# Optimization experiments

Measured on AMD Instinct MI355X. Metric: run time of the kernel, lower is better.

Reference implementation:

```python
import jax, jax.numpy as jnp
import numpy as np

B, S, D = 2, 2048, 1024
H = 16
HD = D // H  # 64, per-head size
EPS = 1e-5


def _ln(x, g, b):
    mu = jnp.mean(x, axis=-1, keepdims=True)
    var = jnp.var(x, axis=-1, keepdims=True)
    return (x - mu) * jax.lax.rsqrt(var + EPS) * g + b


def setup_inputs() -> dict:
    key = jax.random.key(0)
    ks = jax.random.split(key, 8)
    sd = 1.0 / np.sqrt(D)
    return {
        "x": jax.random.normal(ks[0], (B, S, D), jnp.float32),
        "w_qkv": jax.random.normal(ks[1], (3 * D, D), jnp.float32) * sd,
        "w_proj": jax.random.normal(ks[2], (D, D), jnp.float32) * sd,
        "b_proj": jnp.zeros((D,), jnp.float32),
        "w1": jax.random.normal(ks[3], (4 * D, D), jnp.float32) * sd,
        "b1": jnp.zeros((4 * D,), jnp.float32),
        "w2": jax.random.normal(ks[4], (D, 4 * D), jnp.float32) * (1.0 / np.sqrt(4 * D)),
        "b2": jnp.zeros((D,), jnp.float32),
        "ln1_g": jnp.ones((D,), jnp.float32),
        "ln1_b": jnp.zeros((D,), jnp.float32),
        "ln2_g": jnp.ones((D,), jnp.float32),
        "ln2_b": jnp.zeros((D,), jnp.float32),
    }


def reference(x, w_qkv, w_proj, b_proj, w1, b1, w2, b2, ln1_g, ln1_b, ln2_g, ln2_b):
    # --- pre-LN self-attention ---
    h = _ln(x, ln1_g, ln1_b)
    qkv = jnp.einsum("bsd,ed->bse", h, w_qkv)  # [B,S,3D]
    q, k, v = jnp.split(qkv, 3, axis=-1)
    # [B,H,S,HD]
    q = q.reshape(B, S, H, HD).transpose(0, 2, 1, 3)
    k = k.reshape(B, S, H, HD).transpose(0, 2, 1, 3)
    v = v.reshape(B, S, H, HD).transpose(0, 2, 1, 3)
    logits = jnp.einsum("bhqd,bhkd->bhqk", q, k) / np.sqrt(HD)
    probs = jax.nn.softmax(logits, axis=-1)  # no causal mask in non-flash path
    out = jnp.einsum("bhqk,bhkd->bhqd", probs, v)
    out = out.transpose(0, 2, 1, 3).reshape(B, S, D)
    out = jnp.einsum("bsd,ed->bse", out, w_proj) + b_proj
    x = x + out
    # --- pre-LN MLP ---
    h2 = _ln(x, ln2_g, ln2_b)
    h2 = jax.nn.relu(jnp.einsum("bsd,fd->bsf", h2, w1) + b1)
    h2 = jnp.einsum("bsf,df->bsd", h2, w2) + b2
    return x + h2
```

## Files before the change

kernel.cpp:

```cpp
#include <hip/hip_runtime.h>
#include <stdint.h>

typedef unsigned short ushort_t;
typedef __attribute__((ext_vector_type(8))) short s16x8;
typedef __attribute__((ext_vector_type(4))) float f32x4;

static __device__ __forceinline__ float bf2f(ushort_t u) {
  union { unsigned int i; float f; } x; x.i = ((unsigned int)u) << 16; return x.f;
}
static __device__ __forceinline__ ushort_t f2bf(float f) {
  union { float f; unsigned int i; } x; x.f = f;
  unsigned int r = (x.i + 0x7FFFu + ((x.i >> 16) & 1u)) >> 16;
  return (ushort_t)r;
}
static __device__ __forceinline__ unsigned f2bf_pos_u(float f) {
  return (__float_as_uint(f) + 0x8000u) >> 16;
}
static __device__ __forceinline__ bool nonfin(float f) {
  return (__float_as_uint(f) & 0x7F800000u) == 0x7F800000u;
}

static __device__ __forceinline__ float dpp_add16(float x) {
  float y;
  y = __int_as_float(__builtin_amdgcn_update_dpp(0, __float_as_int(x), 0xB1, 0xF, 0xF, true)); x += y;
  y = __int_as_float(__builtin_amdgcn_update_dpp(0, __float_as_int(x), 0x4E, 0xF, 0xF, true)); x += y;
  y = __int_as_float(__builtin_amdgcn_update_dpp(0, __float_as_int(x), 0x141, 0xF, 0xF, true)); x += y;
  y = __int_as_float(__builtin_amdgcn_update_dpp(0, __float_as_int(x), 0x140, 0xF, 0xF, true)); x += y;
  return x;
}

#define GLL16(gp, lp) __builtin_amdgcn_global_load_lds( \
    (const __attribute__((address_space(1))) void*)(gp), \
    (__attribute__((address_space(3))) void*)(lp), 16, 0, 0)

__global__ void zero_flags(int* flags) { if (threadIdx.x < 16) flags[threadIdx.x] = 0; }

__global__ void apply_flags(const int* __restrict__ flags, float* __restrict__ out) {
  int i = threadIdx.x;
  if (i < 7 && flags[i]) out[i] = 1.0e5f * (i + 1);
}

__global__ __launch_bounds__(256) void cvt2(
    const float* __restrict__ a, ushort_t* __restrict__ oa, int na_units,
    const float* __restrict__ b, ushort_t* __restrict__ ob) {
  int u = blockIdx.x * 256 + threadIdx.x;
  const float* in; ushort_t* out; size_t off;
  if (u < na_units) { in = a; out = oa; off = (size_t)u * 8; }
  else              { in = b; out = ob; off = (size_t)(u - na_units) * 8; }
  f32x4 x0 = *(const f32x4*)(in + off);
  f32x4 x1 = *(const f32x4*)(in + off + 4);
  s16x8 o;
#pragma unroll
  for (int j = 0; j < 4; j++) { o[j] = f2bf(x0[j]); o[4 + j] = f2bf(x1[j]); }
  *(s16x8*)(out + off) = o;
}

__global__ __launch_bounds__(256) void ln_kernel(
    const float* __restrict__ x, const float* __restrict__ g,
    const float* __restrict__ b, ushort_t* __restrict__ o,
    int* __restrict__ flags, int flag_idx) {
  int row = blockIdx.x;
  int tid = threadIdx.x;
  const float* xr = x + (size_t)row * 1024;
  f32x4 v = *(const f32x4*)(xr + tid * 4);
  float s = 0.f, ss = 0.f;
#pragma unroll
  for (int j = 0; j < 4; j++) { s += v[j]; ss += v[j] * v[j]; }
#pragma unroll
  for (int off = 32; off > 0; off >>= 1) {
    s += __shfl_xor(s, off);
    ss += __shfl_xor(ss, off);
  }
  __shared__ float red[8];
  int wave = tid >> 6, lane = tid & 63;
  if (lane == 0) { red[wave] = s; red[4 + wave] = ss; }
  __syncthreads();
  s = red[0] + red[1] + red[2] + red[3];
  ss = red[4] + red[5] + red[6] + red[7];
  float mu = s * (1.f / 1024.f);
  float var = ss * (1.f / 1024.f) - mu * mu;
  float rstd = rsqrtf(var + 1e-5f);
  f32x4 gg = *(const f32x4*)(g + tid * 4);
  f32x4 bb = *(const f32x4*)(b + tid * 4);
  ushort_t* orow = o + (size_t)row * 1024 + tid * 4;
#pragma unroll
  for (int j = 0; j < 4; j++) {
    float vv = (v[j] - mu) * rstd * gg[j] + bb[j];
    if (nonfin(vv)) { atomicOr(flags + flag_idx, 1); vv = 0.f; }
    orow[j] = f2bf(vv);
  }
}

template <int BM, int EPI>
__global__ __launch_bounds__(256) void gemm_bt(
    const ushort_t* __restrict__ A, const ushort_t* __restrict__ Bt,
    const float* __restrict__ bias, const float* __restrict__ res,
    ushort_t* __restrict__ Cb, float* __restrict__ Cf,
    int M, int N, int K, int lda, int ldb) {
  constexpr int AM = BM / 32;
  __shared__ ushort_t sA[BM * 32];
  __shared__ ushort_t sB[128 * 32];
  int tid = threadIdx.x;
  int wave = tid >> 6, lane = tid & 63;
  int wm = wave >> 1, wn = wave & 1;
  int bm = blockIdx.x, bn = blockIdx.y;
  int g = lane >> 4, r = lane & 15;

  int e0 = wave * 1024 + lane * 8;
  int e1 = e0 + 512;
  const ushort_t* gB0 = Bt + (size_t)(bn * 128 + (e0 >> 5)) * ldb + (e0 & 31);
  const ushort_t* gB1 = Bt + (size_t)(bn * 128 + (e1 >> 5)) * ldb + (e1 & 31);
  ushort_t* lB0 = sB + wave * 1024;
  ushort_t* lB1 = sB + wave * 1024 + 512;
  int ea = (BM == 128) ? e0 : (wave * 512 + lane * 8);
  const ushort_t* gA0 = A + (size_t)(bm * BM + (ea >> 5)) * lda + (ea & 31);
  const ushort_t* gA1 = A + (size_t)(bm * BM + (e1 >> 5)) * lda + (e1 & 31);
  ushort_t* lA0 = sA + ((BM == 128) ? wave * 1024 : wave * 512);
  ushort_t* lA1 = sA + wave * 1024 + 512;

  f32x4 acc[AM][4];
#pragma unroll
  for (int m = 0; m < AM; m++)
#pragma unroll
    for (int n = 0; n < 4; n++) acc[m][n] = (f32x4){0.f, 0.f, 0.f, 0.f};

  for (int k0 = 0; k0 < K; k0 += 32) {
    GLL16(gA0, lA0);
    if constexpr (BM == 128) GLL16(gA1, lA1);
    GLL16(gB0, lB0);
    GLL16(gB1, lB1);
    gA0 += 32; gB0 += 32; gB1 += 32;
    if constexpr (BM == 128) gA1 += 32;
    __syncthreads();
    s16x8 af[AM], bfr[4];
#pragma unroll
    for (int m = 0; m < AM; m++)
      af[m] = *(const s16x8*)&sA[(wm * (BM / 2) + m * 16 + r) * 32 + g * 8];
#pragma unroll
    for (int n = 0; n < 4; n++)
      bfr[n] = *(const s16x8*)&sB[(wn * 64 + n * 16 + r) * 32 + g * 8];
#pragma unroll
    for (int m = 0; m < AM; m++)
#pragma unroll
      for (int n = 0; n < 4; n++)
        acc[m][n] = __builtin_amdgcn_mfma_f32_16x16x32_bf16(af[m], bfr[n], acc[m][n], 0, 0, 0);
    __syncthreads();
  }

#pragma unroll
  for (int n = 0; n < 4; n++) {
    int colg = bn * 128 + wn * 64 + n * 16 + r;
    float bv = (EPI == 2 || EPI == 6) ? bias[colg] : 0.f;
#pragma unroll
    for (int m = 0; m < AM; m++) {
#pragma unroll
      for (int q = 0; q < 4; q++) {
        int rowg = bm * BM + wm * (BM / 2) + m * 16 + g * 4 + q;
        size_t idx = (size_t)rowg * N + colg;
        float vv = acc[m][n][q] + bv;
        if (EPI == 2) vv = fmaxf(vv, 0.f);
        if (EPI == 6) vv += res[idx];
        if (EPI == 9) vv += Cf[idx];
        if (EPI == 6 || EPI == 9) Cf[idx] = vv;
        else Cb[idx] = f2bf(vv);
      }
    }
  }
}

__global__ __launch_bounds__(256) void attn_kernel(
    const ushort_t* __restrict__ qkv, ushort_t* __restrict__ out,
    int* __restrict__ flags) {
  __shared__ ushort_t sK[2][64 * 72];
  __shared__ ushort_t sVt[2][64 * 72];
  __shared__ ushort_t sP[128 * 72];
  int tid = threadIdx.x, wave = tid >> 6, lane = tid & 63;
  int g = lane >> 4, r = lane & 15;
  int bh = blockIdx.x, qt = blockIdx.y;
  int b = bh >> 4, h = bh & 15;
  const ushort_t* base = qkv + (size_t)b * 2048 * 3072 + h * 64;
  const ushort_t* qb = base;
  const ushort_t* kb = base + 1024;
  const ushort_t* vb = base + 2048;
  int q0 = qt * 128;
  const float SC = 0.125f * 1.44269504f;

  int srow = tid >> 3;
  int scol = (tid & 7) * 8;

  s16x8 aq[2][2];
#pragma unroll
  for (int t = 0; t < 2; t++)
#pragma unroll
    for (int hh = 0; hh < 2; hh++)
      aq[t][hh] = *(const s16x8*)(qb + (size_t)(q0 + wave * 32 + t * 16 + r) * 3072 + hh * 32 + g * 8);

  f32x4 O[2][4];
  float l_r[2][4];
#pragma unroll
  for (int t = 0; t < 2; t++)
#pragma unroll
    for (int n = 0; n < 4; n++) O[t][n] = (f32x4){0.f, 0.f, 0.f, 0.f};
#pragma unroll
  for (int t = 0; t < 2; t++)
#pragma unroll
    for (int qq = 0; qq < 4; qq++) l_r[t][qq] = 0.f;

  {
    const ushort_t* kr = kb + (size_t)srow * 3072 + scol;
    s16x8 k0 = *(const s16x8*)kr;
    s16x8 k1 = *(const s16x8*)(kr + (size_t)32 * 3072);
    const ushort_t* vp = vb + (size_t)srow * 3072 + scol;
    s16x8 v0 = *(const s16x8*)vp;
    s16x8 v1 = *(const s16x8*)(vp + (size_t)32 * 3072);
    *(s16x8*)&sK[0][srow * 72 + scol] = k0;
    *(s16x8*)&sK[0][(srow + 32) * 72 + scol] = k1;
#pragma unroll
    for (int j = 0; j < 8; j++) {
      unsigned w = ((unsigned)(unsigned short)v0[j]) | (((unsigned)(unsigned short)v1[j]) << 16);
      *(unsigned*)&sVt[0][(scol + j) * 72 + srow * 2] = w;
    }
  }

  for (int kt = 0; kt < 32; ++kt) {
    int cur = kt & 1;
    __syncthreads();

    s16x8 nk0 = {}, nk1 = {}, nv0 = {}, nv1 = {};
    if (kt < 31) {
      int kv0n = (kt + 1) * 64;
      const ushort_t* kr = kb + (size_t)(kv0n + srow) * 3072 + scol;
      nk0 = *(const s16x8*)kr;
      nk1 = *(const s16x8*)(kr + (size_t)32 * 3072);
      const ushort_t* vp = vb + (size_t)(kv0n + srow) * 3072 + scol;
      nv0 = *(const s16x8*)vp;
      nv1 = *(const s16x8*)(vp + (size_t)32 * 3072);
    }

    f32x4 sc[2][4];
    __builtin_amdgcn_s_setprio(1);
#pragma unroll
    for (int n = 0; n < 4; n++) {
      s16x8 bk0 = *(const s16x8*)&sK[cur][(n * 16 + r) * 72 + g * 8];
      s16x8 bk1 = *(const s16x8*)&sK[cur][(n * 16 + r) * 72 + 32 + g * 8];
#pragma unroll
      for (int t = 0; t < 2; t++) {
        f32x4 z = (f32x4){0.f, 0.f, 0.f, 0.f};
        z = __builtin_amdgcn_mfma_f32_16x16x32_bf16(aq[t][0], bk0, z, 0, 0, 0);
        z = __builtin_amdgcn_mfma_f32_16x16x32_bf16(aq[t][1], bk1, z, 0, 0, 0);
        sc[t][n] = z;
      }
    }
    __builtin_amdgcn_s_setprio(0);

    if (kt < 31) {
      *(s16x8*)&sK[cur ^ 1][srow * 72 + scol] = nk0;
      *(s16x8*)&sK[cur ^ 1][(srow + 32) * 72 + scol] = nk1;
#pragma unroll
      for (int j = 0; j < 8; j++) {
        unsigned w = ((unsigned)(unsigned short)nv0[j]) | (((unsigned)(unsigned short)nv1[j]) << 16);
        *(unsigned*)&sVt[cur ^ 1][(scol + j) * 72 + srow * 2] = w;
      }
    }

#pragma unroll
    for (int t = 0; t < 2; t++) {
#pragma unroll
      for (int qq = 0; qq < 4; qq++) {
        float p0 = exp2f(sc[t][0][qq] * SC);
        float p1 = exp2f(sc[t][1][qq] * SC);
        float p2 = exp2f(sc[t][2][qq] * SC);
        float p3 = exp2f(sc[t][3][qq] * SC);
        l_r[t][qq] += (p0 + p1) + (p2 + p3);
        int qr = wave * 32 + t * 16 + g * 4 + qq;
        *(unsigned*)&sP[qr * 72 + 2 * r]      = f2bf_pos_u(p0) | (f2bf_pos_u(p2) << 16);
        *(unsigned*)&sP[qr * 72 + 32 + 2 * r] = f2bf_pos_u(p1) | (f2bf_pos_u(p3) << 16);
      }
    }

    s16x8 pa[2][2];
#pragma unroll
    for (int t = 0; t < 2; t++) {
      int qr2 = wave * 32 + t * 16 + r;
      pa[t][0] = *(const s16x8*)&sP[qr2 * 72 + g * 8];
      pa[t][1] = *(const s16x8*)&sP[qr2 * 72 + 32 + g * 8];
    }
    __builtin_amdgcn_s_setprio(1);
#pragma unroll
    for (int n = 0; n < 4; n++) {
      int dd = n * 16 + r;
      s16x8 bv0 = *(const s16x8*)&sVt[cur][dd * 72 + g * 8];
      s16x8 bv1 = *(const s16x8*)&sVt[cur][dd * 72 + 32 + g * 8];
#pragma unroll
      for (int t = 0; t < 2; t++) {
        O[t][n] = __builtin_amdgcn_mfma_f32_16x16x32_bf16(pa[t][0], bv0, O[t][n], 0, 0, 0);
        O[t][n] = __builtin_amdgcn_mfma_f32_16x16x32_bf16(pa[t][1], bv1, O[t][n], 0, 0, 0);
      }
    }
    __builtin_amdgcn_s_setprio(0);
  }

#pragma unroll
  for (int t = 0; t < 2; t++) {
#pragma unroll
    for (int qq = 0; qq < 4; qq++) {
      float li = 1.f / dpp_add16(l_r[t][qq]);
#pragma unroll
      for (int n = 0; n < 4; n++) {
        float vv = O[t][n][qq] * li;
        if (nonfin(vv)) { atomicOr(flags + 3, 1); vv = 0.f; }
        int rowg = b * 2048 + q0 + wave * 32 + t * 16 + g * 4 + qq;
        int colg = h * 64 + n * 16 + r;
        out[(size_t)rowg * 1024 + colg] = f2bf(vv);
      }
    }
  }
}

extern "C" void kernel_launch(void* const* d_in, const int* in_sizes, int n_in,
                              void* d_out, int out_size, void* d_ws, size_t ws_size,
                              hipStream_t stream) {
  const float* x      = (const float*)d_in[0];
  const float* w_qkv  = (const float*)d_in[1];
  const float* w_proj = (const float*)d_in[2];
  const float* b_proj = (const float*)d_in[3];
  const float* w1     = (const float*)d_in[4];
  const float* b1     = (const float*)d_in[5];
  const float* w2     = (const float*)d_in[6];
  const float* b2     = (const float*)d_in[7];
  const float* ln1g   = (const float*)d_in[8];
  const float* ln1b   = (const float*)d_in[9];
  const float* ln2g   = (const float*)d_in[10];
  const float* ln2b   = (const float*)d_in[11];
  float* outp = (float*)d_out;
  char* wsb = (char*)d_ws;

  const size_t MB = 1024 * 1024;
  int*      flags  = (int*)wsb;
  ushort_t* wqkvb  = (ushort_t*)(wsb + 1 * MB);
  ushort_t* wprojb = (ushort_t*)(wsb + 7 * MB);
  ushort_t* h1     = (ushort_t*)(wsb + 9 * MB);
  ushort_t* qkv    = (ushort_t*)(wsb + 17 * MB);
  ushort_t* attnb  = (ushort_t*)(wsb + 41 * MB);
  ushort_t* h2     = (ushort_t*)(wsb + 1 * MB);
  ushort_t* w1b    = (ushort_t*)(wsb + 9 * MB);
  ushort_t* w2b    = (ushort_t*)(wsb + 17 * MB);
  ushort_t* hmid   = (ushort_t*)(wsb + 25 * MB);
  bool single_mlp = (ws_size >= 57 * MB);

  dim3 blk(256);
  zero_flags<<<dim3(1), dim3(64), 0, stream>>>(flags);

  cvt2<<<dim3(2048), blk, 0, stream>>>(w_qkv, wqkvb, 393216, w_proj, wprojb);
  ln_kernel<<<dim3(4096), blk, 0, stream>>>(x, ln1g, ln1b, h1, flags, 0);
  gemm_bt<128, 0><<<dim3(32, 24), blk, 0, stream>>>(h1, wqkvb, nullptr, nullptr, qkv, nullptr,
                                                    4096, 3072, 1024, 1024, 1024);
  attn_kernel<<<dim3(32, 16), blk, 0, stream>>>(qkv, attnb, flags);

  cvt2<<<dim3(4096), blk, 0, stream>>>(w1, w1b, 524288, w2, w2b);

  gemm_bt<64, 6><<<dim3(64, 8), blk, 0, stream>>>(attnb, wprojb, b_proj, x, nullptr, outp,
                                                  4096, 1024, 1024, 1024, 1024);

  ln_kernel<<<dim3(4096), blk, 0, stream>>>(outp, ln2g, ln2b, h2, flags, 1);
  if (single_mlp) {
    gemm_bt<128, 2><<<dim3(32, 32), blk, 0, stream>>>(h2, w1b, b1, nullptr, hmid, nullptr,
                                                      4096, 4096, 1024, 1024, 1024);
    gemm_bt<64, 6><<<dim3(64, 8), blk, 0, stream>>>(hmid, w2b, b2, outp, nullptr, outp,
                                                    4096, 1024, 4096, 4096, 4096);
  } else {
    for (int fc = 0; fc < 2; ++fc) {
      gemm_bt<128, 2><<<dim3(32, 16), blk, 0, stream>>>(
          h2, w1b + (size_t)fc * 2048 * 1024, b1 + fc * 2048, nullptr, hmid, nullptr,
          4096, 2048, 1024, 1024, 1024);
      if (fc == 0)
        gemm_bt<64, 6><<<dim3(64, 8), blk, 0, stream>>>(
            hmid, w2b + fc * 2048, b2, outp, nullptr, outp,
            4096, 1024, 2048, 2048, 4096);
      else
        gemm_bt<64, 9><<<dim3(64, 8), blk, 0, stream>>>(
            hmid, w2b + fc * 2048, nullptr, nullptr, nullptr, outp,
            4096, 1024, 2048, 2048, 4096);
    }
  }
  apply_flags<<<dim3(1), dim3(64), 0, stream>>>(flags, outp);
}
```

Baseline: 296.9 us.

## Double GEMM K-tile to 64 with XOR-swizzled LDS layout

The GEMM main loop now stages a 64-wide K slice per iteration instead of 32, which halves the number of barrier pairs and global-to-LDS load rounds per output tile. The LDS layout is XOR-swizzled on the column by row&7, applied on the global source address, so the 128-byte rows no longer cause bank conflicts on the fragment reads. This doubles shared memory use per block, which may reduce occupancy.

```diff
diff --git a/kernel.cpp b/kernel.cpp
--- a/kernel.cpp
+++ b/kernel.cpp
@@ -98,25 +98,34 @@
     ushort_t* __restrict__ Cb, float* __restrict__ Cf,
     int M, int N, int K, int lda, int ldb) {
   constexpr int AM = BM / 32;
-  __shared__ ushort_t sA[BM * 32];
-  __shared__ ushort_t sB[128 * 32];
+  constexpr int ACH = (BM * 64) / (256 * 8);
+  __shared__ ushort_t sA[BM * 64];
+  __shared__ ushort_t sB[128 * 64];
   int tid = threadIdx.x;
   int wave = tid >> 6, lane = tid & 63;
   int wm = wave >> 1, wn = wave & 1;
   int bm = blockIdx.x, bn = blockIdx.y;
   int g = lane >> 4, r = lane & 15;
-
-  int e0 = wave * 1024 + lane * 8;
-  int e1 = e0 + 512;
-  const ushort_t* gB0 = Bt + (size_t)(bn * 128 + (e0 >> 5)) * ldb + (e0 & 31);
-  const ushort_t* gB1 = Bt + (size_t)(bn * 128 + (e1 >> 5)) * ldb + (e1 & 31);
-  ushort_t* lB0 = sB + wave * 1024;
-  ushort_t* lB1 = sB + wave * 1024 + 512;
-  int ea = (BM == 128) ? e0 : (wave * 512 + lane * 8);
-  const ushort_t* gA0 = A + (size_t)(bm * BM + (ea >> 5)) * lda + (ea & 31);
-  const ushort_t* gA1 = A + (size_t)(bm * BM + (e1 >> 5)) * lda + (e1 & 31);
-  ushort_t* lA0 = sA + ((BM == 128) ? wave * 1024 : wave * 512);
-  ushort_t* lA1 = sA + wave * 1024 + 512;
+  int rx8 = (r & 7) << 3;
+
+  const ushort_t* gA[ACH];
+  ushort_t* lA[ACH];
+#pragma unroll
+  for (int c = 0; c < ACH; c++) {
+    int e = wave * (BM * 16) + c * 512 + lane * 8;
+    int row = e >> 6, col = e & 63;
+    gA[c] = A + (size_t)(bm * BM + row) * lda + (col ^ ((row & 7) << 3));
+    lA[c] = sA + wave * (BM * 16) + c * 512;
+  }
+  const ushort_t* gB[4];
+  ushort_t* lB[4];
+#pragma unroll
+  for (int c = 0; c < 4; c++) {
+    int e = wave * 2048 + c * 512 + lane * 8;
+    int row = e >> 6, col = e & 63;
+    gB[c] = Bt + (size_t)(bn * 128 + row) * ldb + (col ^ ((row & 7) << 3));
+    lB[c] = sB + wave * 2048 + c * 512;
+  }
 
   f32x4 acc[AM][4];
 #pragma unroll
@@ -124,26 +133,28 @@
 #pragma unroll
     for (int n = 0; n < 4; n++) acc[m][n] = (f32x4){0.f, 0.f, 0.f, 0.f};
 
-  for (int k0 = 0; k0 < K; k0 += 32) {
-    GLL16(gA0, lA0);
-    if constexpr (BM == 128) GLL16(gA1, lA1);
-    GLL16(gB0, lB0);
-    GLL16(gB1, lB1);
-    gA0 += 32; gB0 += 32; gB1 += 32;
-    if constexpr (BM == 128) gA1 += 32;
+  for (int k0 = 0; k0 < K; k0 += 64) {
+#pragma unroll
+    for (int c = 0; c < ACH; c++) { GLL16(gA[c], lA[c]); gA[c] += 64; }
+#pragma unroll
+    for (int c = 0; c < 4; c++) { GLL16(gB[c], lB[c]); gB[c] += 64; }
     __syncthreads();
-    s16x8 af[AM], bfr[4];
-#pragma unroll
-    for (int m = 0; m < AM; m++)
-      af[m] = *(const s16x8*)&sA[(wm * (BM / 2) + m * 16 + r) * 32 + g * 8];
-#pragma unroll
-    for (int n = 0; n < 4; n++)
-      bfr[n] = *(const s16x8*)&sB[(wn * 64 + n * 16 + r) * 32 + g * 8];
-#pragma unroll
-    for (int m = 0; m < AM; m++)
+#pragma unroll
+    for (int kk = 0; kk < 2; kk++) {
+      int cx = (kk * 32 + g * 8) ^ rx8;
+      s16x8 af[AM], bfr[4];
+#pragma unroll
+      for (int m = 0; m < AM; m++)
+        af[m] = *(const s16x8*)&sA[(wm * (BM / 2) + m * 16 + r) * 64 + cx];
 #pragma unroll
       for (int n = 0; n < 4; n++)
-        acc[m][n] = __builtin_amdgcn_mfma_f32_16x16x32_bf16(af[m], bfr[n], acc[m][n], 0, 0, 0);
+        bfr[n] = *(const s16x8*)&sB[(wn * 64 + n * 16 + r) * 64 + cx];
+#pragma unroll
+      for (int m = 0; m < AM; m++)
+#pragma unroll
+        for (int n = 0; n < 4; n++)
+          acc[m][n] = __builtin_amdgcn_mfma_f32_16x16x32_bf16(af[m], bfr[n], acc[m][n], 0, 0, 0);
+    }
     __syncthreads();
   }
 
```

New measurement: 266.9 us. -10.1%, faster.
